# Optimization experiments

Hardware: AMD Instinct MI355X
Metric: run time of the kernel (lower is better)

## Reference

```python
import jax, jax.numpy as jnp
import numpy as np

IMPOSSIBLE = -10000.0
TAGSET_SIZE = 64
NUM_TAGS = TAGSET_SIZE + 2  # C = 66
START_IDX = NUM_TAGS - 2
STOP_IDX = NUM_TAGS - 1
B, L, D = 32, 1024, 1024


def setup_inputs() -> dict:
    key = jax.random.key(0)
    k1, k2, k3, k4, k5 = jax.random.split(key, 5)
    features = jax.random.normal(k1, (B, L, D), dtype=jnp.float32)
    ys = jax.random.randint(k2, (B, L), 0, TAGSET_SIZE).astype(jnp.int64)
    masks = jnp.ones((B, L), dtype=jnp.float32)
    fc_w = jax.random.normal(k3, (D, NUM_TAGS), dtype=jnp.float32) / np.sqrt(D)
    fc_b = jax.random.normal(k4, (NUM_TAGS,), dtype=jnp.float32) * 0.01
    transitions = jax.random.normal(k5, (NUM_TAGS, NUM_TAGS), dtype=jnp.float32)
    # transitions TO start and FROM stop are impossible (torch indexing [to, from])
    transitions = transitions.at[START_IDX, :].set(IMPOSSIBLE)
    transitions = transitions.at[:, STOP_IDX].set(IMPOSSIBLE)
    return {"features": features, "ys": ys, "masks": masks,
            "fc_w": fc_w, "fc_b": fc_b, "transitions": transitions}


def _forward_algorithm(feats, masks, transitions):
    """CRF partition function. feats: [B,L,C], masks: [B,L] -> [B]."""
    Bb, Ll, C = feats.shape
    scores0 = jnp.full((Bb, C), IMPOSSIBLE, dtype=feats.dtype).at[:, START_IDX].set(0.0)

    def step(scores, xs):
        emit_t, m_t = xs  # emit_t: [B,C], m_t: [B]
        # score_t[b, j] = logsumexp_i( scores[b,i] + trans[j,i] + emit[b,j] )
        score_t = jax.nn.logsumexp(
            scores[:, None, :] + transitions[None, :, :] + emit_t[:, :, None], axis=-1)
        scores = score_t * m_t[:, None] + scores * (1.0 - m_t[:, None])
        return scores, None

    xs = (jnp.swapaxes(feats, 0, 1), jnp.swapaxes(masks, 0, 1))  # [L,B,C], [L,B]
    scores, _ = jax.lax.scan(step, scores0, xs)
    return jax.nn.logsumexp(scores + transitions[STOP_IDX][None, :], axis=-1)


def _score_sentence(feats, tags, masks, transitions):
    """Score of the gold tag path. feats: [B,L,C], tags: [B,L] -> [B]."""
    Bb, Ll, C = feats.shape
    emit = jnp.take_along_axis(feats, tags[:, :, None], axis=2)[:, :, 0]  # [B,L]
    start = jnp.full((Bb, 1), START_IDX, dtype=tags.dtype)
    tags_ext = jnp.concatenate([start, tags], axis=1)  # [B,L+1]
    trans_sc = transitions[tags_ext[:, 1:], tags_ext[:, :-1]]  # [B,L]
    lengths = masks.sum(1).astype(jnp.int32)  # [B]
    last_tag = tags_ext[jnp.arange(Bb), lengths]  # [B]
    last_score = transitions[STOP_IDX, last_tag]
    return ((trans_sc + emit) * masks).sum(1) + last_score


def reference(features, ys, masks, fc_w, fc_b, transitions):
    feats = jnp.einsum('bld,dc->blc', features, fc_w) + fc_b  # [B,L,C]
    masks_ = masks.astype(feats.dtype)
    forward_score = _forward_algorithm(feats, masks_, transitions)  # [B]
    gold_score = _score_sentence(feats, ys.astype(jnp.int32), masks_, transitions)  # [B]
    return (forward_score, gold_score)
```

## Files before the change

### kernel.cpp

```cpp
#include <hip/hip_runtime.h>
#include <hip/hip_bf16.h>
#include <stdint.h>


#define START_IDX 64
#define STOP_IDX 65
#define LN2F 0.6931471805599453f

typedef __attribute__((ext_vector_type(4))) float f32x4;
typedef __attribute__((ext_vector_type(16))) float f32x16;
typedef __attribute__((ext_vector_type(8))) __bf16 bf16x8;
typedef __attribute__((ext_vector_type(2))) __bf16 bf16x2;
typedef __attribute__((ext_vector_type(4))) int i32x4;

__device__ __forceinline__ void gload_lds16(const void* g, void* l) {
  __builtin_amdgcn_global_load_lds(
      (const __attribute__((address_space(1))) void*)g,
      (__attribute__((address_space(3))) void*)l, 16, 0, 0);
}

__device__ __forceinline__ int pack_bf16(float lo, float hi) {
  bf16x2 t;
  t[0] = (__bf16)lo;
  t[1] = (__bf16)hi;
  return __builtin_bit_cast(int, t);
}

__device__ __forceinline__ void pl32_swap(int& x, int& y) {
  asm("v_permlane32_swap_b32 %0, %1" : "+v"(x), "+v"(y));
}

template <int CTRL>
__device__ __forceinline__ float dpp_mov(float v) {
  return __int_as_float(
      __builtin_amdgcn_update_dpp(0, __float_as_int(v), CTRL, 0xF, 0xF, true));
}
__device__ __forceinline__ float wave_max64(float v) {
  v = fmaxf(v, dpp_mov<0xB1>(v));
  v = fmaxf(v, dpp_mov<0x4E>(v));
  v = fmaxf(v, dpp_mov<0x141>(v));
  v = fmaxf(v, dpp_mov<0x140>(v));
  v = fmaxf(v, dpp_mov<0x142>(v));
  v = fmaxf(v, dpp_mov<0x143>(v));
  return v;
}
__device__ __forceinline__ float wave_sum64(float v) {
  v += dpp_mov<0xB1>(v);
  v += dpp_mov<0x4E>(v);
  v += dpp_mov<0x141>(v);
  v += dpp_mov<0x140>(v);
  v += dpp_mov<0x142>(v);
  v += dpp_mov<0x143>(v);
  return v;
}

__global__ __launch_bounds__(256) void crf_wcvt(const float* __restrict__ W,
                                                unsigned short* __restrict__ Wbt) {
  __shared__ float tile[64][65];
  const int t = threadIdx.x;
  const int kb = blockIdx.x;
#pragma unroll
  for (int i = 0; i < 16; ++i) {
    const int f = i * 256 + t;
    const int k = f >> 6, n = f & 63;
    tile[k][n] = W[(kb * 64 + k) * 66 + n];
  }
  __syncthreads();
#pragma unroll
  for (int i = 0; i < 16; ++i) {
    const int f = i * 256 + t;
    const int n = f >> 6, k = f & 63;
    union { __bf16 h; unsigned short u; } cv;
    cv.h = (__bf16)tile[k][n];
    Wbt[n * 1024 + kb * 64 + k] = cv.u;
  }
}

__global__ __launch_bounds__(256, 2) void crf_fwd(const float* __restrict__ features,
                                                  const unsigned short* __restrict__ Wbt,
                                                  const float* __restrict__ bias,
                                                  const float* __restrict__ masks,
                                                  const float* __restrict__ trans,
                                                  float* __restrict__ featsOut,
                                                  float* __restrict__ chunkP,
                                                  int* __restrict__ chunkExp) {
  __shared__ __align__(16) char smem[49152];
  const int tid = threadIdx.x;
  const int w = tid >> 6, lane = tid & 63, g = lane >> 4, q = lane & 15;
  const int c = blockIdx.x, b = blockIdx.y;

  {
    const float* Abase = features + ((size_t)b << 20) + ((size_t)c << 16);
    const int arow0 = 16 * w + (lane >> 4);
    const int acolb = (lane & 15) * 16;
    const int brow0 = 16 * w + (lane >> 3);
    const int bcolb = (lane & 7) * 16;

    f32x4 acc[4];
#pragma unroll
    for (int nt = 0; nt < 4; ++nt) acc[nt] = (f32x4){0.f, 0.f, 0.f, 0.f};

#pragma unroll
    for (int j = 0; j < 4; ++j) {
      const int row = arow0 + 4 * j;
      gload_lds16((const char*)(Abase + (size_t)row * 1024) +
                      (acolb ^ ((row & 7) << 4)),
                  smem + (16 * w + 4 * j) * 256);
    }
#pragma unroll
    for (int j = 0; j < 2; ++j) {
      const int n = brow0 + 8 * j;
      gload_lds16((const char*)(Wbt + (size_t)n * 1024) +
                      (bcolb ^ ((n & 7) << 4)),
                  smem + 32768 + (16 * w + 8 * j) * 128);
    }

    const int sA = (q & 7) << 4;
    for (int kt = 0; kt < 16; ++kt) {
      const int buf = kt & 1;
      __syncthreads();
      if (kt < 15) {
        const int k0 = (kt + 1) * 64;
#pragma unroll
        for (int j = 0; j < 4; ++j) {
          const int row = arow0 + 4 * j;
          gload_lds16((const char*)(Abase + (size_t)row * 1024 + k0) +
                          (acolb ^ ((row & 7) << 4)),
                      smem + (buf ^ 1) * 16384 + (16 * w + 4 * j) * 256);
        }
#pragma unroll
        for (int j = 0; j < 2; ++j) {
          const int n = brow0 + 8 * j;
          gload_lds16((const char*)(Wbt + (size_t)n * 1024 + k0) +
                          (bcolb ^ ((n & 7) << 4)),
                      smem + 32768 + (buf ^ 1) * 8192 + (16 * w + 8 * j) * 128);
        }
      }
      const char* Ab = smem + buf * 16384 + (16 * w + q) * 256;
      const char* Bb = smem + 32768 + buf * 8192;
#pragma unroll
      for (int kk = 0; kk < 2; ++kk) {
        float4 alo = *(const float4*)(Ab + ((kk * 128 + 32 * g) ^ sA));
        float4 ahi = *(const float4*)(Ab + ((kk * 128 + 32 * g + 16) ^ sA));
        bf16x8 af;
        af[0] = (__bf16)alo.x; af[1] = (__bf16)alo.y;
        af[2] = (__bf16)alo.z; af[3] = (__bf16)alo.w;
        af[4] = (__bf16)ahi.x; af[5] = (__bf16)ahi.y;
        af[6] = (__bf16)ahi.z; af[7] = (__bf16)ahi.w;
#pragma unroll
        for (int nt = 0; nt < 4; ++nt) {
          const int n = q + 16 * nt;
          bf16x8 bf = *(const bf16x8*)(Bb + n * 128 +
                                       ((kk * 64 + 16 * g) ^ ((n & 7) << 4)));
          acc[nt] = __builtin_amdgcn_mfma_f32_16x16x32_bf16(af, bf, acc[nt], 0, 0, 0);
        }
      }
    }
    const float bb0 = bias[q + 0], bb1 = bias[q + 16];
    const float bb2 = bias[q + 32], bb3 = bias[q + 48];
    float (*expE)[64] = (float(*)[64])smem;
#pragma unroll
    for (int r = 0; r < 4; ++r) {
      const int tl = 16 * w + 4 * g + r;
      float* orow = featsOut + (((size_t)(b << 10) + (c << 6) + tl) << 6) + q;
      const float v0 = acc[0][r] + bb0, v1 = acc[1][r] + bb1;
      const float v2 = acc[2][r] + bb2, v3 = acc[3][r] + bb3;
      orow[0] = v0; orow[16] = v1; orow[32] = v2; orow[48] = v3;
      expE[tl][q + 0]  = __expf(v0);
      expE[tl][q + 16] = __expf(v1);
      expE[tl][q + 32] = __expf(v2);
      expE[tl][q + 48] = __expf(v3);
    }
  }
  __syncthreads();

  const int n32 = lane & 31, H = lane >> 5;
  const int hc = w >> 1;
  const int hcol = w & 1;
  const int cc = 2 * c + hc;
  const int tbase = cc << 5;

  bf16x8 Ea[2][4];
#pragma unroll
  for (int a = 0; a < 2; ++a) {
    const float* tp = trans + (size_t)(32 * a + n32) * 66 + 8 * H;
#pragma unroll
    for (int kc = 0; kc < 4; ++kc)
#pragma unroll
      for (int e = 0; e < 8; ++e)
        Ea[a][kc][e] = (__bf16)__expf(tp[16 * kc + e]);
  }

  float pv[2][16];
#pragma unroll
  for (int a = 0; a < 2; ++a)
#pragma unroll
    for (int r = 0; r < 16; ++r) {
      const int row = 32 * a + (r & 3) + 8 * (r >> 2) + 4 * H;
      pv[a][r] = (row == 32 * hcol + n32) ? 1.f : 0.f;
    }

  const float* mb = masks + (b << 10);
  int tmi = tbase + n32; if (tmi > 1023) tmi = 1023;
  const float mkv = mb[tmi];

  f32x16 zz;
#pragma unroll
  for (int i = 0; i < 16; ++i) zz[i] = 0.f;

  float wmx = 1.f;
  int e_acc = 0;
  float (*expE)[64] = (float(*)[64])smem;
  const int ts0 = (cc == 0) ? 1 : 0;

  for (int ts = ts0; ts < 32; ++ts) {
    const float m =
        __int_as_float(__builtin_amdgcn_readlane(__float_as_int(mkv), ts));
    if (m == 0.f) continue;
    const int tl = (hc << 5) + ts;

    int ex = 0; float sc = 1.f;
    if ((ts & 1) == 0) {
      const int mxb = __builtin_amdgcn_readlane(__float_as_int(wmx), 63);
      ex = ((mxb >> 23) & 0xFF) - 127;
      sc = __int_as_float((127 - ex) << 23);
    }

    f32x4 ce[2][4];
#pragma unroll
    for (int a = 0; a < 2; ++a)
#pragma unroll
      for (int u = 0; u < 4; ++u)
        ce[a][u] = *(const f32x4*)&expE[tl][32 * a + 8 * u + 4 * H];

    int pk0[8], pk1[8];
#pragma unroll
    for (int mi = 0; mi < 8; ++mi) {
      pk0[mi] = pack_bf16(pv[0][2 * mi], pv[0][2 * mi + 1]);
      pk1[mi] = pack_bf16(pv[1][2 * mi], pv[1][2 * mi + 1]);
    }

    f32x16 a0, a1;
#pragma unroll
    for (int kc = 0; kc < 4; ++kc) {
      int* pks = (kc >> 1) ? pk1 : pk0;
      const int bs = 4 * (kc & 1);
      int x0 = pks[bs + 0], y0 = pks[bs + 2];
      int x1 = pks[bs + 1], y1 = pks[bs + 3];
      pl32_swap(x0, y0);
      pl32_swap(x1, y1);
      i32x4 bi = {x0, x1, y0, y1};
      bf16x8 B = __builtin_bit_cast(bf16x8, bi);
      if (kc == 0) {
        a0 = __builtin_amdgcn_mfma_f32_32x32x16_bf16(Ea[0][0], B, zz, 0, 0, 0);
        a1 = __builtin_amdgcn_mfma_f32_32x32x16_bf16(Ea[1][0], B, zz, 0, 0, 0);
      } else {
        a0 = __builtin_amdgcn_mfma_f32_32x32x16_bf16(Ea[0][kc], B, a0, 0, 0, 0);
        a1 = __builtin_amdgcn_mfma_f32_32x32x16_bf16(Ea[1][kc], B, a1, 0, 0, 0);
      }
    }

    float nmx = 0.f;
    if (m == 1.f) {
#pragma unroll
      for (int u = 0; u < 4; ++u)
#pragma unroll
        for (int vv = 0; vv < 4; ++vv) {
          const int r = 4 * u + vv;
          const float v0 = a0[r] * ce[0][u][vv] * sc;
          const float v1 = a1[r] * ce[1][u][vv] * sc;
          pv[0][r] = v0; pv[1][r] = v1;
          nmx = fmaxf(nmx, fmaxf(v0, v1));
        }
    } else {
#pragma unroll
      for (int u = 0; u < 4; ++u)
#pragma unroll
        for (int vv = 0; vv < 4; ++vv) {
          const int r = 4 * u + vv;
          float v0 = a0[r] * ce[0][u][vv] * sc;
          float v1 = a1[r] * ce[1][u][vv] * sc;
          v0 = m * v0 + (1.f - m) * sc * pv[0][r];
          v1 = m * v1 + (1.f - m) * sc * pv[1][r];
          pv[0][r] = v0; pv[1][r] = v1;
          nmx = fmaxf(nmx, fmaxf(v0, v1));
        }
    }
    if (ts & 1) wmx = wave_max64(nmx);
    e_acc += ex;
  }

  float* Pb = chunkP + (((size_t)(b * 32 + cc)) << 12) + 32 * hcol;
#pragma unroll
  for (int a = 0; a < 2; ++a)
#pragma unroll
    for (int r = 0; r < 16; ++r) {
      const int row = 32 * a + (r & 3) + 8 * (r >> 2) + 4 * H;
      Pb[(size_t)row * 64 + n32] = pv[a][r];
    }
  if (lane == 0) chunkExp[((b * 32 + cc) << 1) + hcol] = e_acc;
}

__global__ void crf_fin(const float* __restrict__ feats,
                        const int* __restrict__ ys,
                        const float* __restrict__ masks,
                        const float* __restrict__ trans,
                        const float* __restrict__ chunkP,
                        const int* __restrict__ chunkExp,
                        float* __restrict__ out) {
  __shared__ __align__(16) float vb[64];
  const int lane = threadIdx.x;
  const int b = blockIdx.x >> 1;
  if ((blockIdx.x & 1) == 0) {
    float v = __expf(feats[((size_t)b << 16) + lane]) *
              __expf(trans[lane * 66 + START_IDX]);
    int e_acc = 0;
    for (int cc = 0; cc < 32; ++cc) {
      const int E0 = chunkExp[((b * 32 + cc) << 1)];
      const int E1 = chunkExp[((b * 32 + cc) << 1) + 1];
      const int Em = (E0 > E1) ? E0 : E1;
      int sh = 127 + ((lane < 32) ? E0 : E1) - Em;
      if (sh < 1) sh = 1;
      vb[lane] = v * __int_as_float(sh << 23);
      __builtin_amdgcn_wave_barrier();
      const float* Pr = chunkP + (((size_t)(b * 32 + cc)) << 12) + (size_t)lane * 64;
      float q0 = 0.f, q1 = 0.f, q2 = 0.f, q3 = 0.f;
#pragma unroll
      for (int j4 = 0; j4 < 16; ++j4) {
        float4 p = *(const float4*)(Pr + 4 * j4);
        float4 x = ((const float4*)vb)[j4];
        q0 = fmaf(p.x, x.x, q0); q1 = fmaf(p.y, x.y, q1);
        q2 = fmaf(p.z, x.z, q2); q3 = fmaf(p.w, x.w, q3);
      }
      const float qq = (q0 + q1) + (q2 + q3);
      float mx = wave_max64(qq);
      mx = __int_as_float(__builtin_amdgcn_readlane(__float_as_int(mx), 63));
      const int ex = ((__float_as_int(mx) >> 23) & 0xFF) - 127;
      v = qq * __int_as_float((127 - ex) << 23);
      e_acc += ex + Em;
      __builtin_amdgcn_wave_barrier();
    }
    const float sum = wave_sum64(v * __expf(trans[STOP_IDX * 66 + lane]));
    const float s =
        __int_as_float(__builtin_amdgcn_readlane(__float_as_int(sum), 63));
    if (lane == 0) out[b] = __logf(s) + (float)e_acc * LN2F;
  } else {
    const float* fb = feats + ((size_t)b << 16);
    const float* mb = masks + (b << 10);
    const int* yb = ys + (b << 10);
    float s = 0.f, cnt = 0.f;
#pragma unroll
    for (int cc = 0; cc < 16; ++cc) {
      const int t = cc * 64 + lane;
      const float m = mb[t];
      const int y = yb[t];
      const int yp = (t == 0) ? START_IDX : yb[t - 1];
      s += (trans[y * 66 + yp] + fb[t * 64 + y]) * m;
      cnt += m;
    }
    float tot = wave_sum64(s);
    float len = wave_sum64(cnt);
    int totb = __builtin_amdgcn_readlane(__float_as_int(tot), 63);
    int lenb = __builtin_amdgcn_readlane(__float_as_int(len), 63);
    if (lane == 0) {
      const int Lr = (int)__int_as_float(lenb);
      const int last = (Lr == 0) ? START_IDX : yb[Lr - 1];
      out[32 + b] = __int_as_float(totb) + trans[STOP_IDX * 66 + last];
    }
  }
}

extern "C" void kernel_launch(void* const* d_in, const int* in_sizes, int n_in,
                              void* d_out, int out_size, void* d_ws, size_t ws_size,
                              hipStream_t stream) {
  const float* features = (const float*)d_in[0];
  const int* ys         = (const int*)d_in[1];
  const float* masks    = (const float*)d_in[2];
  const float* fc_w     = (const float*)d_in[3];
  const float* fc_b     = (const float*)d_in[4];
  const float* trans    = (const float*)d_in[5];
  float* outp = (float*)d_out;

  char* ws = (char*)d_ws;
  float* feats_ws = (float*)ws;
  unsigned short* Wbt = (unsigned short*)(ws + 8388608);
  float* chunkP = (float*)(ws + 8388608 + 131072);
  int* chunkExp = (int*)(ws + 8388608 + 131072 + 16777216);

  crf_wcvt<<<16, 256, 0, stream>>>(fc_w, Wbt);
  dim3 cg(16, 32);
  crf_fwd<<<cg, 256, 0, stream>>>(features, Wbt, fc_b, masks, trans,
                                  feats_ws, chunkP, chunkExp);
  crf_fin<<<64, 64, 0, stream>>>(feats_ws, ys, masks, trans, chunkP, chunkExp, outp);
}
```

Before: 266.7 us.

## Split fused GEMM+scan kernel into triple-buffered GEMM and separate scan kernel

```diff
diff --git a/kernel.cpp b/kernel.cpp
--- a/kernel.cpp
+++ b/kernel.cpp
@@ -76,100 +76,117 @@
   }
 }
 
-__global__ __launch_bounds__(256, 2) void crf_fwd(const float* __restrict__ features,
-                                                  const unsigned short* __restrict__ Wbt,
-                                                  const float* __restrict__ bias,
-                                                  const float* __restrict__ masks,
-                                                  const float* __restrict__ trans,
-                                                  float* __restrict__ featsOut,
-                                                  float* __restrict__ chunkP,
-                                                  int* __restrict__ chunkExp) {
-  __shared__ __align__(16) char smem[49152];
+__global__ __launch_bounds__(256) void crf_mm(const float* __restrict__ A,
+                                              const unsigned short* __restrict__ Wbt,
+                                              const float* __restrict__ bias,
+                                              float* __restrict__ out) {
+  __shared__ __align__(16) char smem[73728];
   const int tid = threadIdx.x;
   const int w = tid >> 6, lane = tid & 63, g = lane >> 4, q = lane & 15;
+  const size_t blk = blockIdx.x;
+  const float* Abase = A + (blk << 16);
+
+  const int arow = 16 * w + (lane >> 4);
+  const int acolb = (lane & 15) * 16;
+  const int brow = 16 * w + (lane >> 3);
+  const int bcolb = (lane & 7) * 16;
+
+  auto stage = [&](int kt, int buf) {
+    char* Ad = smem + buf * 24576;
+    char* Bd = Ad + 16384;
+    const int k0 = kt << 6;
+#pragma unroll
+    for (int j = 0; j < 4; ++j) {
+      const int row = arow + 4 * j;
+      gload_lds16((const char*)(Abase + (size_t)row * 1024 + k0) +
+                      (acolb ^ ((row & 7) << 4)),
+                  Ad + (16 * w + 4 * j) * 256);
+    }
+#pragma unroll
+    for (int j = 0; j < 2; ++j) {
+      const int n = brow + 8 * j;
+      gload_lds16((const char*)(Wbt + (size_t)n * 1024 + k0) +
+                      (bcolb ^ ((n & 7) << 4)),
+                  Bd + (16 * w + 8 * j) * 128);
+    }
+  };
+
+  f32x4 acc[4];
+#pragma unroll
+  for (int nt = 0; nt < 4; ++nt) acc[nt] = (f32x4){0.f, 0.f, 0.f, 0.f};
+
+  stage(0, 0);
+  stage(1, 1);
+
+  const int sA = (q & 7) << 4;
+  for (int kt = 0; kt < 16; ++kt) {
+    const int buf = kt % 3;
+    if (kt < 14) stage(kt + 2, (kt + 2) % 3);
+    if (kt < 14)
+      asm volatile("s_waitcnt vmcnt(12)" ::: "memory");
+    else if (kt == 14)
+      asm volatile("s_waitcnt vmcnt(6)" ::: "memory");
+    else
+      asm volatile("s_waitcnt vmcnt(0)" ::: "memory");
+    __builtin_amdgcn_sched_barrier(0);
+    __builtin_amdgcn_s_barrier();
+    const char* Ab = smem + buf * 24576 + (16 * w + q) * 256;
+    const char* Bb = smem + buf * 24576 + 16384;
+#pragma unroll
+    for (int kk = 0; kk < 2; ++kk) {
+      float4 alo = *(const float4*)(Ab + ((kk * 128 + 32 * g) ^ sA));
+      float4 ahi = *(const float4*)(Ab + ((kk * 128 + 32 * g + 16) ^ sA));
+      bf16x8 af;
+      af[0] = (__bf16)alo.x; af[1] = (__bf16)alo.y;
+      af[2] = (__bf16)alo.z; af[3] = (__bf16)alo.w;
+      af[4] = (__bf16)ahi.x; af[5] = (__bf16)ahi.y;
+      af[6] = (__bf16)ahi.z; af[7] = (__bf16)ahi.w;
+#pragma unroll
+      for (int nt = 0; nt < 4; ++nt) {
+        const int n = q + 16 * nt;
+        bf16x8 bfv = *(const bf16x8*)(Bb + n * 128 +
+                                      ((kk * 64 + 16 * g) ^ ((n & 7) << 4)));
+        acc[nt] = __builtin_amdgcn_mfma_f32_16x16x32_bf16(af, bfv, acc[nt], 0, 0, 0);
+      }
+    }
+    __builtin_amdgcn_sched_barrier(0);
+    __builtin_amdgcn_s_barrier();
+  }
+
+  const float bb0 = bias[q + 0], bb1 = bias[q + 16];
+  const float bb2 = bias[q + 32], bb3 = bias[q + 48];
+#pragma unroll
+  for (int r = 0; r < 4; ++r) {
+    const int tl = 16 * w + 4 * g + r;
+    float* orow = out + ((blk << 6) + tl) * 64 + q;
+    orow[0]  = acc[0][r] + bb0;
+    orow[16] = acc[1][r] + bb1;
+    orow[32] = acc[2][r] + bb2;
+    orow[48] = acc[3][r] + bb3;
+  }
+}
+
+__global__ __launch_bounds__(256) void crf_scan(const float* __restrict__ feats,
+                                                const float* __restrict__ masks,
+                                                const float* __restrict__ trans,
+                                                float* __restrict__ chunkP,
+                                                int* __restrict__ chunkExp) {
+  __shared__ __align__(16) float expE[64][64];
+  const int tid = threadIdx.x;
+  const int w = tid >> 6, lane = tid & 63;
   const int c = blockIdx.x, b = blockIdx.y;
 
   {
-    const float* Abase = features + ((size_t)b << 20) + ((size_t)c << 16);
-    const int arow0 = 16 * w + (lane >> 4);
-    const int acolb = (lane & 15) * 16;
-    const int brow0 = 16 * w + (lane >> 3);
-    const int bcolb = (lane & 7) * 16;
-
-    f32x4 acc[4];
-#pragma unroll
-    for (int nt = 0; nt < 4; ++nt) acc[nt] = (f32x4){0.f, 0.f, 0.f, 0.f};
-
-#pragma unroll
-    for (int j = 0; j < 4; ++j) {
-      const int row = arow0 + 4 * j;
-      gload_lds16((const char*)(Abase + (size_t)row * 1024) +
-                      (acolb ^ ((row & 7) << 4)),
-                  smem + (16 * w + 4 * j) * 256);
-    }
-#pragma unroll
-    for (int j = 0; j < 2; ++j) {
-      const int n = brow0 + 8 * j;
-      gload_lds16((const char*)(Wbt + (size_t)n * 1024) +
-                      (bcolb ^ ((n & 7) << 4)),
-                  smem + 32768 + (16 * w + 8 * j) * 128);
-    }
-
-    const int sA = (q & 7) << 4;
-    for (int kt = 0; kt < 16; ++kt) {
-      const int buf = kt & 1;
-      __syncthreads();
-      if (kt < 15) {
-        const int k0 = (kt + 1) * 64;
-#pragma unroll
-        for (int j = 0; j < 4; ++j) {
-          const int row = arow0 + 4 * j;
-          gload_lds16((const char*)(Abase + (size_t)row * 1024 + k0) +
-                          (acolb ^ ((row & 7) << 4)),
-                      smem + (buf ^ 1) * 16384 + (16 * w + 4 * j) * 256);
-        }
-#pragma unroll
-        for (int j = 0; j < 2; ++j) {
-          const int n = brow0 + 8 * j;
-          gload_lds16((const char*)(Wbt + (size_t)n * 1024 + k0) +
-                          (bcolb ^ ((n & 7) << 4)),
-                      smem + 32768 + (buf ^ 1) * 8192 + (16 * w + 8 * j) * 128);
-        }
-      }
-      const char* Ab = smem + buf * 16384 + (16 * w + q) * 256;
-      const char* Bb = smem + 32768 + buf * 8192;
-#pragma unroll
-      for (int kk = 0; kk < 2; ++kk) {
-        float4 alo = *(const float4*)(Ab + ((kk * 128 + 32 * g) ^ sA));
-        float4 ahi = *(const float4*)(Ab + ((kk * 128 + 32 * g + 16) ^ sA));
-        bf16x8 af;
-        af[0] = (__bf16)alo.x; af[1] = (__bf16)alo.y;
-        af[2] = (__bf16)alo.z; af[3] = (__bf16)alo.w;
-        af[4] = (__bf16)ahi.x; af[5] = (__bf16)ahi.y;
-        af[6] = (__bf16)ahi.z; af[7] = (__bf16)ahi.w;
-#pragma unroll
-        for (int nt = 0; nt < 4; ++nt) {
-          const int n = q + 16 * nt;
-          bf16x8 bf = *(const bf16x8*)(Bb + n * 128 +
-                                       ((kk * 64 + 16 * g) ^ ((n & 7) << 4)));
-          acc[nt] = __builtin_amdgcn_mfma_f32_16x16x32_bf16(af, bf, acc[nt], 0, 0, 0);
-        }
-      }
-    }
-    const float bb0 = bias[q + 0], bb1 = bias[q + 16];
-    const float bb2 = bias[q + 32], bb3 = bias[q + 48];
-    float (*expE)[64] = (float(*)[64])smem;
-#pragma unroll
-    for (int r = 0; r < 4; ++r) {
-      const int tl = 16 * w + 4 * g + r;
-      float* orow = featsOut + (((size_t)(b << 10) + (c << 6) + tl) << 6) + q;
-      const float v0 = acc[0][r] + bb0, v1 = acc[1][r] + bb1;
-      const float v2 = acc[2][r] + bb2, v3 = acc[3][r] + bb3;
-      orow[0] = v0; orow[16] = v1; orow[32] = v2; orow[48] = v3;
-      expE[tl][q + 0]  = __expf(v0);
-      expE[tl][q + 16] = __expf(v1);
-      expE[tl][q + 32] = __expf(v2);
-      expE[tl][q + 48] = __expf(v3);
+    const f32x4* src = (const f32x4*)(feats + (((size_t)(b << 10) + (c << 6)) << 6));
+    f32x4* dst = (f32x4*)expE;
+#pragma unroll
+    for (int i = 0; i < 4; ++i) {
+      const int idx = i * 256 + tid;
+      f32x4 v = src[idx];
+      f32x4 e;
+      e[0] = __expf(v[0]); e[1] = __expf(v[1]);
+      e[2] = __expf(v[2]); e[3] = __expf(v[3]);
+      dst[idx] = e;
     }
   }
   __syncthreads();
@@ -210,7 +227,6 @@
 
   float wmx = 1.f;
   int e_acc = 0;
-  float (*expE)[64] = (float(*)[64])smem;
   const int ts0 = (cc == 0) ? 1 : 0;
 
   for (int ts = ts0; ts < 32; ++ts) {
@@ -250,13 +266,13 @@
       pl32_swap(x0, y0);
       pl32_swap(x1, y1);
       i32x4 bi = {x0, x1, y0, y1};
-      bf16x8 B = __builtin_bit_cast(bf16x8, bi);
+      bf16x8 Bf = __builtin_bit_cast(bf16x8, bi);
       if (kc == 0) {
-        a0 = __builtin_amdgcn_mfma_f32_32x32x16_bf16(Ea[0][0], B, zz, 0, 0, 0);
-        a1 = __builtin_amdgcn_mfma_f32_32x32x16_bf16(Ea[1][0], B, zz, 0, 0, 0);
+        a0 = __builtin_amdgcn_mfma_f32_32x32x16_bf16(Ea[0][0], Bf, zz, 0, 0, 0);
+        a1 = __builtin_amdgcn_mfma_f32_32x32x16_bf16(Ea[1][0], Bf, zz, 0, 0, 0);
       } else {
-        a0 = __builtin_amdgcn_mfma_f32_32x32x16_bf16(Ea[0][kc], B, a0, 0, 0, 0);
-        a1 = __builtin_amdgcn_mfma_f32_32x32x16_bf16(Ea[1][kc], B, a1, 0, 0, 0);
+        a0 = __builtin_amdgcn_mfma_f32_32x32x16_bf16(Ea[0][kc], Bf, a0, 0, 0, 0);
+        a1 = __builtin_amdgcn_mfma_f32_32x32x16_bf16(Ea[1][kc], Bf, a1, 0, 0, 0);
       }
     }
 
@@ -388,8 +404,8 @@
   int* chunkExp = (int*)(ws + 8388608 + 131072 + 16777216);
 
   crf_wcvt<<<16, 256, 0, stream>>>(fc_w, Wbt);
+  crf_mm<<<512, 256, 0, stream>>>(features, Wbt, fc_b, feats_ws);
   dim3 cg(16, 32);
-  crf_fwd<<<cg, 256, 0, stream>>>(features, Wbt, fc_b, masks, trans,
-                                  feats_ws, chunkP, chunkExp);
+  crf_scan<<<cg, 256, 0, stream>>>(feats_ws, masks, trans, chunkP, chunkExp);
   crf_fin<<<64, 64, 0, stream>>>(feats_ws, ys, masks, trans, chunkP, chunkExp, outp);
 }
```

New measurement: 276.4 us. 3.6% more time.
